# Optimization experiments

Measured on AMD Instinct MI355X. Metric: run time of the kernel, lower is better.

Reference implementation:

```python
import jax, jax.numpy as jnp
import numpy as np

N, C, T, V, D = 128, 64, 256, 25, 64  # batch(*persons), in_ch, frames, joints, out_ch
RED = 4  # SE reduction


def _shift_indices(c, d, v):
    i = np.arange(v)[:, None]
    j = np.arange(c)[None, :]
    shift_in = ((i * c + j + j * c) % (c * v)).reshape(-1)
    jd = np.arange(d)[None, :]
    shift_out = ((i * d + jd - jd * d) % (d * v)).reshape(-1)
    return jnp.asarray(shift_in, jnp.int32), jnp.asarray(shift_out, jnp.int32)


def setup_inputs() -> dict:
    key = jax.random.key(0)
    ks = jax.random.split(key, 6)
    r = C // RED
    x0 = jax.random.normal(ks[0], (N, C, T, V), jnp.float32)
    fc1_w = jax.random.normal(ks[1], (r, C), jnp.float32) * (2.0 / C) ** 0.5
    fc1_b = jnp.zeros((r,), jnp.float32)
    fc2_w = jax.random.normal(ks[2], (4, r), jnp.float32) * (2.0 / r) ** 0.5
    fc2_b = jnp.zeros((4,), jnp.float32)
    W = jax.random.normal(ks[3], (4, C, D), jnp.float32) * (1.0 / D) ** 0.5
    b = jnp.zeros((4, D), jnp.float32)
    mask = jax.random.normal(ks[4], (1, V, C), jnp.float32) * 0.1  # Feature_Mask
    gamma = jnp.ones((V * D,), jnp.float32)
    beta = jnp.zeros((V * D,), jnp.float32)
    shift_in, shift_out = _shift_indices(C, D, V)
    return dict(x0=x0, epoch=100, fc1_w=fc1_w, fc1_b=fc1_b, fc2_w=fc2_w,
                fc2_b=fc2_b, W=W, b=b, mask=mask, gamma=gamma, beta=beta,
                shift_in=shift_in, shift_out=shift_out)


def reference(x0, epoch, fc1_w, fc1_b, fc2_w, fc2_b, W, b, mask, gamma, beta,
              shift_in, shift_out):
    n, c, t, v = x0.shape
    d = W.shape[-1]
    # DY_SEModule: global avg pool -> 1x1 conv -> relu -> 1x1 conv -> softmax(/tao)
    pooled = x0.mean(axis=(2, 3))                       # [n, c]
    h = jax.nn.relu(pooled @ fc1_w.T + fc1_b)           # [n, c//4]
    logits = h @ fc2_w.T + fc2_b                        # [n, 4]
    tao = 1.0 if epoch >= 60 else -(30.0 - 1.0) / 60.0 * epoch + 30.0
    gate = jax.nn.softmax(logits / tao, axis=1)         # [n, 4]
    # per-sample fused weights/bias
    Wf = jnp.einsum('kcd,nk->ncd', W, gate)             # [n, c, d]
    bf = jnp.einsum('kc,nk->nc', b, gate)               # [n, d]
    # shift-in gather + tanh feature mask
    x = x0.transpose(0, 2, 3, 1).reshape(n * t, v * c)  # [n*t, v*c]
    x = jnp.take(x, shift_in, axis=1).reshape(n * t, v, c)
    x = x * (jnp.tanh(mask) + 1.0)
    x = x.reshape(n, t, v, c)
    # per-sample linear
    x = jnp.einsum('ntvc,ncd->ntvd', x, Wf) + bf[:, None, None, :]
    # shift-out gather + BatchNorm1d over v*d features (training-mode stats)
    x = jnp.take(x.reshape(n * t, v * d), shift_out, axis=1)
    mu = x.mean(axis=0)
    var = x.var(axis=0)
    x = (x - mu) * jax.lax.rsqrt(var + 1e-5) * gamma + beta
    x = x.reshape(n, t, v, d).transpose(0, 3, 1, 2)     # [n, d, t, v]
    # residual (in==out -> identity down) + relu
    return jax.nn.relu(x + x0)
```

## Files before the change

### kernel.cpp

```cpp
#include <hip/hip_runtime.h>
#include <hip/hip_bf16.h>
#include <math.h>

#define N_   128
#define C_   64
#define T_   256
#define V_   25
#define D_   64
#define CTV  409600
#define TV   6400

typedef __attribute__((ext_vector_type(8))) short short8;
typedef __attribute__((ext_vector_type(4))) short short4v;
typedef __attribute__((ext_vector_type(4))) float f32x4;

__device__ inline unsigned short f2b(float f) {
    __hip_bfloat16 h = __float2bfloat16(f);
    return *(unsigned short*)&h;
}
__device__ inline float b2f(unsigned short u) {
    return __uint_as_float(((unsigned)u) << 16);
}

__global__ __launch_bounds__(256) void k_pool(const float* __restrict__ x0,
                                              float* __restrict__ pooled) {
    const int bid = blockIdx.x;
    const int tid = threadIdx.x;
    const float4* base = (const float4*)(x0 + (size_t)bid * TV);
    float s = 0.f;
    for (int i = tid; i < 1600; i += 256) {
        float4 f = base[i];
        s += (f.x + f.y) + (f.z + f.w);
    }
    #pragma unroll
    for (int off = 32; off > 0; off >>= 1) s += __shfl_down(s, off);
    __shared__ float red[4];
    if ((tid & 63) == 0) red[tid >> 6] = s;
    __syncthreads();
    if (tid == 0) pooled[bid] = (red[0] + red[1] + red[2] + red[3]) * (1.0f / TV);
}

__global__ __launch_bounds__(256) void k_se(
    const float* __restrict__ pooled, const float* __restrict__ fc1w,
    const float* __restrict__ fc1b,  const float* __restrict__ fc2w,
    const float* __restrict__ fc2b,  const float* __restrict__ Wm,
    const float* __restrict__ bm,    const float* __restrict__ mask,
    const int* __restrict__ ep,
    unsigned short* __restrict__ Wfb, float* __restrict__ bfv,
    unsigned short* __restrict__ mgT)
{
    __shared__ float sp[64], sh[16], sl[4];
    __shared__ float wk[64 * 65];
    const int tid = threadIdx.x, n = blockIdx.x;
    if (tid < 64) sp[tid] = pooled[n * 64 + tid];
    __syncthreads();
    if (tid < 16) {
        float s = fc1b[tid];
        #pragma unroll
        for (int c = 0; c < 64; c++) s = fmaf(sp[c], fc1w[tid * 64 + c], s);
        sh[tid] = fmaxf(s, 0.f);
    }
    __syncthreads();
    if (tid < 4) {
        float s = fc2b[tid];
        #pragma unroll
        for (int j = 0; j < 16; j++) s = fmaf(sh[j], fc2w[tid * 16 + j], s);
        sl[tid] = s;
    }
    __syncthreads();
    const int e = ep[0];
    const float tao = (e >= 60) ? 1.0f : (-(29.0f / 60.0f) * (float)e + 30.0f);
    const float it = 1.0f / tao;
    float l0 = sl[0] * it, l1 = sl[1] * it, l2 = sl[2] * it, l3 = sl[3] * it;
    float mx = fmaxf(fmaxf(l0, l1), fmaxf(l2, l3));
    float e0 = expf(l0 - mx), e1 = expf(l1 - mx), e2 = expf(l2 - mx), e3 = expf(l3 - mx);
    float inv = 1.0f / (e0 + e1 + e2 + e3);
    float ga[4] = {e0 * inv, e1 * inv, e2 * inv, e3 * inv};

    float accW[16];
    #pragma unroll
    for (int m = 0; m < 16; m++) accW[m] = 0.f;
    #pragma unroll
    for (int k = 0; k < 4; k++) {
        __syncthreads();
        for (int i = tid; i < 4096; i += 256)
            wk[(i >> 6) * 65 + (i & 63)] = Wm[k * 4096 + i];
        __syncthreads();
        #pragma unroll
        for (int m = 0; m < 16; m++) {
            int o = m * 256 + tid;
            int w  = o >> 10, s = (o >> 9) & 1;
            int ln = (o >> 3) & 63, j = o & 7;
            int c  = s * 32 + (ln >> 4) * 8 + j;
            int d  = w * 16 + (ln & 15);
            accW[m] = fmaf(ga[k], wk[c * 65 + d], accW[m]);
        }
    }
    #pragma unroll
    for (int m = 0; m < 16; m++)
        Wfb[(size_t)n * 4096 + m * 256 + tid] = f2b(accW[m]);
    if (tid < 64)
        bfv[n * 64 + tid] = ga[0] * bm[tid] + ga[1] * bm[64 + tid] +
                            ga[2] * bm[128 + tid] + ga[3] * bm[192 + tid];
    if (n == 0) {
        for (int i = tid; i < 1600; i += 256) {
            int c = i / 25, v = i - c * 25;
            mgT[i] = f2b(tanhf(mask[v * 64 + c]) + 1.0f);
        }
    }
}

__global__ __launch_bounds__(256, 4) void k_main(
    const float* __restrict__ x0, const unsigned short* __restrict__ Wfb,
    const float* __restrict__ bfv, const unsigned short* __restrict__ mgT,
    __hip_bfloat16* __restrict__ y, float* __restrict__ sn)
{
    __shared__ unsigned short At[2][7616];
    __shared__ unsigned short mgTs[64 * 26];

    const int tid = threadIdx.x;
    const int w = tid >> 6, l = tid & 63, q = l >> 4, m = l & 15;
    const int n = blockIdx.x >> 4;
    const int tbase = (blockIdx.x & 15) * 16;

    short8 bf0 = *(const short8*)(Wfb + (size_t)n * 4096 + (w * 2 + 0) * 512 + l * 8);
    short8 bf1 = *(const short8*)(Wfb + (size_t)n * 4096 + (w * 2 + 1) * 512 + l * 8);
    const int d = w * 16 + m;
    const float bfl = bfv[n * 64 + d];

    for (int i = tid; i < 1600; i += 256) {
        int c = i / 25, v = i - c * 25;
        mgTs[c * 26 + v] = mgT[i];
    }
    for (int i = tid; i < 816; i += 256) {
        int b = (i >= 408) ? 1 : 0;
        int ii = i - b * 408;
        int rr = ii / 34, wo = ii - rr * 34;
        int t = rr / 3, vr = rr - t * 3 + 1;
        ((unsigned*)At[b])[(96 + t * 4 + vr) * 34 + wo] = 0u;
    }
    __syncthreads();

    float ss[25], sq[25];
    #pragma unroll
    for (int v = 0; v < 25; v++) { ss[v] = 0.f; sq[v] = 0.f; }

    const float4* src = (const float4*)x0;
    for (int sub = 0; sub < 4; sub++) {
        const int t0 = tbase + sub * 4;
        unsigned short* Ab = At[sub & 1];
        const int fb = n * 102400 + (t0 * 25) / 4;
        for (int i = tid; i < 1600; i += 256) {
            int c = i / 25, r = i - c * 25;
            float4 f = src[fb + c * 1600 + r];
            int cm = c; if (cm >= 25) cm -= 25; if (cm >= 25) cm -= 25;
            int f0 = r * 4;
            int t = f0 / 25;
            int vp = f0 - t * 25;
            int v = vp - cm; if (v < 0) v += 25;
            #pragma unroll
            for (int e = 0; e < 4; e++) {
                float xv = (e == 0) ? f.x : (e == 1) ? f.y : (e == 2) ? f.z : f.w;
                int rho = (v >> 2) * 16 + t * 4 + (v & 3);
                Ab[rho * 68 + c] = f2b(xv * b2f(mgTs[c * 26 + v]));
                vp++; v++;
                if (vp == 25) { vp = 0; t++; }
                if (v == 25) v = 0;
            }
        }
        __syncthreads();
        #pragma unroll
        for (int tau = 0; tau < 7; tau++) {
            const unsigned short* Abr = Ab + (tau * 16 + m) * 68 + q * 8;
            short4v a0l = *(const short4v*)(Abr);
            short4v a0h = *(const short4v*)(Abr + 4);
            short4v a1l = *(const short4v*)(Abr + 32);
            short4v a1h = *(const short4v*)(Abr + 36);
            short8 a0 = {a0l[0],a0l[1],a0l[2],a0l[3],a0h[0],a0h[1],a0h[2],a0h[3]};
            short8 a1 = {a1l[0],a1l[1],a1l[2],a1l[3],a1h[0],a1h[1],a1h[2],a1h[3]};
            f32x4 acc = {0.f, 0.f, 0.f, 0.f};
            acc = __builtin_amdgcn_mfma_f32_16x16x32_bf16(a0, bf0, acc, 0, 0, 0);
            acc = __builtin_amdgcn_mfma_f32_16x16x32_bf16(a1, bf1, acc, 0, 0, 0);
            const int t = t0 + q;
            __hip_bfloat16* yb = y + ((size_t)(n * T_ + t) * 25) * 64 + d;
            #pragma unroll
            for (int r = 0; r < 4; r++) {
                const int v = tau * 4 + r;
                if (v < 25) {
                    float val = acc[r] + bfl;
                    yb[v * 64] = __float2bfloat16(val);
                    ss[v] += val;
                    sq[v] = fmaf(val, val, sq[v]);
                }
            }
        }
    }
    #pragma unroll
    for (int v = 0; v < 25; v++) {
        ss[v] += __shfl_xor(ss[v], 16); ss[v] += __shfl_xor(ss[v], 32);
        sq[v] += __shfl_xor(sq[v], 16); sq[v] += __shfl_xor(sq[v], 32);
    }
    if (q == 0) {
        float* sb = sn + (size_t)n * 3200;
        #pragma unroll
        for (int v = 0; v < 25; v++) {
            atomicAdd(&sb[v * 64 + d], ss[v]);
            atomicAdd(&sb[1600 + v * 64 + d], sq[v]);
        }
    }
}

__global__ __launch_bounds__(256) void k_bn(
    const float* __restrict__ sn,
    const float* __restrict__ gamma, const float* __restrict__ beta,
    const int* __restrict__ shout,
    float2* __restrict__ ab)
{
    const int tid = threadIdx.x;
    const int jl = tid >> 2;
    const int p  = tid & 3;
    const int j = blockIdx.x * 64 + jl;
    const int src = shout[j];
    float s = 0.f, qq = 0.f;
    for (int nn = p; nn < 128; nn += 4) {
        s  += sn[(size_t)nn * 3200 + src];
        qq += sn[(size_t)nn * 3200 + 1600 + src];
    }
    s  += __shfl_xor(s, 1);  s  += __shfl_xor(s, 2);
    qq += __shfl_xor(qq, 1); qq += __shfl_xor(qq, 2);
    if (p == 0) {
        const float invn = 1.0f / 32768.0f;
        float mu = s * invn;
        float var = qq * invn - mu * mu;
        float rstd = rsqrtf(var + 1e-5f);
        float a = gamma[j] * rstd;
        float bb = beta[j] - mu * a;
        int dd = j & 63, vo = j >> 6;
        ab[dd * 25 + vo] = make_float2(a, bb);
    }
}

__global__ __launch_bounds__(256, 6) void k_out(
    const __hip_bfloat16* __restrict__ y, const float* __restrict__ x0,
    const float2* __restrict__ ab, float* __restrict__ out)
{
    __shared__ __align__(16) unsigned short ys[8 * 1652];
    const int tid = threadIdx.x;
    const int n = blockIdx.x >> 5;
    const int t0 = (blockIdx.x & 31) * 8;
    const uint4* ysrc = (const uint4*)((const unsigned short*)y + (size_t)(n * T_ + t0) * 1600);
    for (int i = tid; i < 1600; i += 256) {
        uint4 g = ysrc[i];
        int tl = i / 200, r8 = (i - tl * 200) * 8;
        int v = r8 >> 6, d0 = r8 & 63;
        unsigned* p = (unsigned*)ys + ((tl * 1652 + v * 66 + d0) >> 1);
        p[0] = g.x; p[1] = g.y; p[2] = g.z; p[3] = g.w;
    }
    __syncthreads();
    const float* xb = x0 + (size_t)n * CTV + t0 * 25;
    float* ob = out + (size_t)n * CTV + t0 * 25;
    for (int o4 = tid; o4 < 3200; o4 += 256) {
        int dd = o4 / 50;
        int rem4 = (o4 - dd * 50) * 4;
        int ddm = dd;
        if (ddm >= 25) ddm -= 25;
        if (ddm >= 25) ddm -= 25;
        int tl = rem4 / 25, vo = rem4 - tl * 25;
        const int base = dd * TV + rem4;
        f32x4 xv = *(const f32x4*)(xb + base);
        f32x4 r;
        #pragma unroll
        for (int e = 0; e < 4; e++) {
            int vy = vo - ddm; if (vy < 0) vy += 25;
            float val = b2f(ys[tl * 1652 + vy * 66 + dd]);
            float2 g = ab[dd * 25 + vo];
            r[e] = fmaxf(fmaf(val, g.x, g.y) + xv[e], 0.f);
            vo++; if (vo == 25) { vo = 0; tl++; }
        }
        __builtin_nontemporal_store(r, (f32x4*)(ob + base));
    }
}

extern "C" void kernel_launch(void* const* d_in, const int* in_sizes, int n_in,
                              void* d_out, int out_size, void* d_ws, size_t ws_size,
                              hipStream_t stream) {
    const float* x0    = (const float*)d_in[0];
    const int*   ep    = (const int*)  d_in[1];
    const float* fc1w  = (const float*)d_in[2];
    const float* fc1b  = (const float*)d_in[3];
    const float* fc2w  = (const float*)d_in[4];
    const float* fc2b  = (const float*)d_in[5];
    const float* Wm    = (const float*)d_in[6];
    const float* bm    = (const float*)d_in[7];
    const float* mask  = (const float*)d_in[8];
    const float* gamma = (const float*)d_in[9];
    const float* beta  = (const float*)d_in[10];
    const int*   shout = (const int*)  d_in[12];
    float* out = (float*)d_out;

    float* wsf = (float*)d_ws;
    float*          pooled = wsf;
    float*          bfv    = wsf + 8192;
    unsigned short* mgT    = (unsigned short*)(wsf + 16384);
    float2*         ab     = (float2*)(wsf + 17984);
    unsigned short* Wfb    = (unsigned short*)(wsf + 22784);
    float*          sn     = wsf + 284928;
    __hip_bfloat16* y      = (__hip_bfloat16*)(wsf + 694528);

    hipMemsetAsync(sn, 0, 409600 * sizeof(float), stream);
    k_pool<<<N_ * C_, 256, 0, stream>>>(x0, pooled);
    k_se<<<N_, 256, 0, stream>>>(pooled, fc1w, fc1b, fc2w, fc2b, Wm, bm, mask,
                                 ep, Wfb, bfv, mgT);
    k_main<<<N_ * 16, 256, 0, stream>>>(x0, Wfb, bfv, mgT, y, sn);
    k_bn<<<25, 256, 0, stream>>>(sn, gamma, beta, shout, ab);
    k_out<<<N_ * 32, 256, 0, stream>>>(y, x0, ab, out);
}
```

Baseline: 573.7 us.

## Software-pipeline x0 loads into double-buffered LDS across MFMA sub-steps

Restructures k_main's sub-tile loop so the global loads and bf16 LDS writes for the next 4-frame tile are issued in register batches interleaved with the MFMA compute of the current tile. The second LDS buffer now actually serves as a double buffer, and the barrier moves to the end of each iteration, leaving one sync per sub-tile. The aim is to hide global memory latency behind compute. In exchange it holds more registers (four float4 prefetch values), which may pressure occupancy at launch bounds of 4 blocks per CU.

```diff
diff --git a/kernel.cpp b/kernel.cpp
--- a/kernel.cpp
+++ b/kernel.cpp
@@ -110,6 +110,26 @@
     }
 }
 
+
+#define LOADIT(dst, it, fb) { int i_ = tid + (it)*256; if (i_ < 1600) { \
+    int c_ = i_ / 25, r_ = i_ - c_ * 25; \
+    dst = src[(fb) + c_ * 1600 + r_]; } }
+
+#define WRITEIT(fsrc, it, AB) { int i_ = tid + (it)*256; if (i_ < 1600) { \
+    int c_ = i_ / 25, r_ = i_ - c_ * 25; \
+    int cm_ = c_; if (cm_ >= 25) cm_ -= 25; if (cm_ >= 25) cm_ -= 25; \
+    int f0_ = r_ * 4; \
+    int t_ = f0_ / 25, vp_ = f0_ - t_ * 25; \
+    int v_ = vp_ - cm_; if (v_ < 0) v_ += 25; \
+    _Pragma("unroll") \
+    for (int e_ = 0; e_ < 4; e_++) { \
+        float xv_ = (e_ == 0) ? fsrc.x : (e_ == 1) ? fsrc.y : (e_ == 2) ? fsrc.z : fsrc.w; \
+        int rho_ = (v_ >> 2) * 16 + t_ * 4 + (v_ & 3); \
+        (AB)[rho_ * 68 + c_] = f2b(xv_ * b2f(mgTs[c_ * 26 + v_])); \
+        vp_++; v_++; \
+        if (vp_ == 25) { vp_ = 0; t_++; } \
+        if (v_ == 25) v_ = 0; } } }
+
 __global__ __launch_bounds__(256, 4) void k_main(
     const float* __restrict__ x0, const unsigned short* __restrict__ Wfb,
     const float* __restrict__ bfv, const unsigned short* __restrict__ mgT,
@@ -146,31 +166,51 @@
     for (int v = 0; v < 25; v++) { ss[v] = 0.f; sq[v] = 0.f; }
 
     const float4* src = (const float4*)x0;
+    const int fb0 = n * 102400 + (tbase * 25) / 4;
+
+    float4 f0, f1, f2, f3;
+    LOADIT(f0, 0, fb0) LOADIT(f1, 1, fb0) LOADIT(f2, 2, fb0) LOADIT(f3, 3, fb0)
+    WRITEIT(f0, 0, At[0]) WRITEIT(f1, 1, At[0]) WRITEIT(f2, 2, At[0]) WRITEIT(f3, 3, At[0])
+    LOADIT(f0, 4, fb0) LOADIT(f1, 5, fb0) LOADIT(f2, 6, fb0)
+    WRITEIT(f0, 4, At[0]) WRITEIT(f1, 5, At[0]) WRITEIT(f2, 6, At[0])
+    __syncthreads();
+
     for (int sub = 0; sub < 4; sub++) {
         const int t0 = tbase + sub * 4;
         unsigned short* Ab = At[sub & 1];
-        const int fb = n * 102400 + (t0 * 25) / 4;
-        for (int i = tid; i < 1600; i += 256) {
-            int c = i / 25, r = i - c * 25;
-            float4 f = src[fb + c * 1600 + r];
-            int cm = c; if (cm >= 25) cm -= 25; if (cm >= 25) cm -= 25;
-            int f0 = r * 4;
-            int t = f0 / 25;
-            int vp = f0 - t * 25;
-            int v = vp - cm; if (v < 0) v += 25;
+        unsigned short* An = At[(sub & 1) ^ 1];
+        const int fbn = fb0 + (sub + 1) * 25;
+        const bool pf = (sub < 3);
+        if (pf) { LOADIT(f0, 0, fbn) LOADIT(f1, 1, fbn) LOADIT(f2, 2, fbn) LOADIT(f3, 3, fbn) }
+        #pragma unroll
+        for (int tau = 0; tau < 4; tau++) {
+            const unsigned short* Abr = Ab + (tau * 16 + m) * 68 + q * 8;
+            short4v a0l = *(const short4v*)(Abr);
+            short4v a0h = *(const short4v*)(Abr + 4);
+            short4v a1l = *(const short4v*)(Abr + 32);
+            short4v a1h = *(const short4v*)(Abr + 36);
+            short8 a0 = {a0l[0],a0l[1],a0l[2],a0l[3],a0h[0],a0h[1],a0h[2],a0h[3]};
+            short8 a1 = {a1l[0],a1l[1],a1l[2],a1l[3],a1h[0],a1h[1],a1h[2],a1h[3]};
+            f32x4 acc = {0.f, 0.f, 0.f, 0.f};
+            acc = __builtin_amdgcn_mfma_f32_16x16x32_bf16(a0, bf0, acc, 0, 0, 0);
+            acc = __builtin_amdgcn_mfma_f32_16x16x32_bf16(a1, bf1, acc, 0, 0, 0);
+            const int t = t0 + q;
+            __hip_bfloat16* yb = y + ((size_t)(n * T_ + t) * 25) * 64 + d;
             #pragma unroll
-            for (int e = 0; e < 4; e++) {
-                float xv = (e == 0) ? f.x : (e == 1) ? f.y : (e == 2) ? f.z : f.w;
-                int rho = (v >> 2) * 16 + t * 4 + (v & 3);
-                Ab[rho * 68 + c] = f2b(xv * b2f(mgTs[c * 26 + v]));
-                vp++; v++;
-                if (vp == 25) { vp = 0; t++; }
-                if (v == 25) v = 0;
+            for (int r = 0; r < 4; r++) {
+                const int v = tau * 4 + r;
+                float val = acc[r] + bfl;
+                yb[v * 64] = __float2bfloat16(val);
+                ss[v] += val;
+                sq[v] = fmaf(val, val, sq[v]);
             }
         }
-        __syncthreads();
-        #pragma unroll
-        for (int tau = 0; tau < 7; tau++) {
+        if (pf) {
+            WRITEIT(f0, 0, An) WRITEIT(f1, 1, An) WRITEIT(f2, 2, An) WRITEIT(f3, 3, An)
+            LOADIT(f0, 4, fbn) LOADIT(f1, 5, fbn) LOADIT(f2, 6, fbn)
+        }
+        #pragma unroll
+        for (int tau = 4; tau < 7; tau++) {
             const unsigned short* Abr = Ab + (tau * 16 + m) * 68 + q * 8;
             short4v a0l = *(const short4v*)(Abr);
             short4v a0h = *(const short4v*)(Abr + 4);
@@ -194,6 +234,8 @@
                 }
             }
         }
+        if (pf) { WRITEIT(f0, 4, An) WRITEIT(f1, 5, An) WRITEIT(f2, 6, An) }
+        __syncthreads();
     }
     #pragma unroll
     for (int v = 0; v < 25; v++) {
```

New measurement: 623.3 us. +8.6%, slower.
